# Performance work log

Hardware: AMD Instinct MI355X
Metric: run time of the kernel (lower is better)

The kernel has to match this reference:

```python
import jax, jax.numpy as jnp
import numpy as np

EPS = 1e-5  # torch BatchNorm1d default eps


def setup_inputs() -> dict:
    key = jax.random.key(0)
    ks = jax.random.split(key, 12)
    B, D, H, R, T = 262144, 128, 64, 32, 8
    return {
        "x": jax.random.normal(ks[0], (B, D), dtype=jnp.float32),
        "t": jax.random.randint(ks[1], (B,), 0, T),
        # shared feature net: Linear(D->H), ReLU, BN(H) [eval mode], Dropout(eval=identity)
        "fw": jax.random.normal(ks[2], (H, D), dtype=jnp.float32) * 0.05,
        "fb": jax.random.normal(ks[3], (H,), dtype=jnp.float32) * 0.05,
        "f_gamma": jnp.ones((H,), jnp.float32),
        "f_beta": jnp.zeros((H,), jnp.float32),
        "f_mean": jax.random.normal(ks[4], (H,), dtype=jnp.float32) * 0.05,
        "f_var": jax.random.uniform(ks[5], (H,), minval=0.5, maxval=1.5),
        # T treatment heads, weights stacked on leading axis:
        # Linear(H->R), ReLU, BN(R), Dropout, Linear(R->1)
        "tw1": jax.random.normal(ks[6], (T, R, H), dtype=jnp.float32) * 0.05,
        "tb1": jax.random.normal(ks[7], (T, R), dtype=jnp.float32) * 0.05,
        "t_gamma": jnp.ones((T, R), jnp.float32),
        "t_beta": jnp.zeros((T, R), jnp.float32),
        "t_mean": jax.random.normal(ks[8], (T, R), dtype=jnp.float32) * 0.05,
        "t_var": jax.random.uniform(ks[9], (T, R), minval=0.5, maxval=1.5),
        "tw2": jax.random.normal(ks[10], (T, R), dtype=jnp.float32) * 0.05,  # [T,1,R] squeezed
        "tb2": jax.random.normal(ks[11], (T,), dtype=jnp.float32) * 0.05,
    }


def reference(x, t, fw, fb, f_gamma, f_beta, f_mean, f_var,
              tw1, tb1, t_gamma, t_beta, t_mean, t_var, tw2, tb2):
    # shared representation: Linear -> ReLU -> BN(eval) -> Dropout(identity)
    h = jax.nn.relu(x @ fw.T + fb)                                     # [B,H]
    h = f_gamma * (h - f_mean) * jax.lax.rsqrt(f_var + EPS) + f_beta   # [B,H]
    # run all T tiny heads densely, then select per-sample head (jit-friendly
    # equivalent of the boolean-mask gather/scatter loop; BN is eval-mode so
    # per-group masking and full-batch compute give identical math)
    z = jnp.einsum('bh,trh->btr', h, tw1) + tb1[None]                  # [B,T,R]
    z = jax.nn.relu(z)
    z = t_gamma[None] * (z - t_mean[None]) * jax.lax.rsqrt(t_var[None] + EPS) + t_beta[None]
    out_all = jnp.einsum('btr,tr->bt', z, tw2) + tb2[None]             # [B,T]
    pred = jnp.take_along_axis(out_all, t[:, None], axis=1)            # [B,1]
    return pred
```

## Files before the change

### kernel.cpp

```cpp
#include <hip/hip_runtime.h>
#include <hip/hip_bf16.h>
#include <cstdint>

#define EPS 1e-5f

typedef short bf16x8 __attribute__((ext_vector_type(8)));
typedef float f32x16 __attribute__((ext_vector_type(16)));
typedef unsigned int u32x4 __attribute__((ext_vector_type(4)));

#define WS_TW1S 0
#define WS_FW   8192
#define WS_TB1Q 12288
#define WS_W2Q  12544
#define WS_FBQ  12800
#define WS_C2   12864

static __device__ __forceinline__ unsigned short f2bf(float f) {
    unsigned int u = __float_as_uint(f);
    u += 0x7fffu + ((u >> 16) & 1u);
    return (unsigned short)(u >> 16);
}
static __device__ __forceinline__ short f2bf_fast(float f) {
    __hip_bfloat16 b = __float2bfloat16(f);
    return __builtin_bit_cast(short, b);
}
static __device__ __forceinline__ unsigned pk_bf16(float lo, float hi) {
    unsigned l = (unsigned)(unsigned short)__builtin_bit_cast(unsigned short, __float2bfloat16(lo));
    unsigned h = (unsigned)(unsigned short)__builtin_bit_cast(unsigned short, __float2bfloat16(hi));
    return l | (h << 16);
}

__global__ void tarnet_pre(
    const float* __restrict__ fw, const float* __restrict__ fb,
    const float* __restrict__ f_gamma, const float* __restrict__ f_beta,
    const float* __restrict__ f_mean,  const float* __restrict__ f_var,
    const float* __restrict__ tw1, const float* __restrict__ tb1,
    const float* __restrict__ t_gamma, const float* __restrict__ t_beta,
    const float* __restrict__ t_mean,  const float* __restrict__ t_var,
    const float* __restrict__ tw2, const float* __restrict__ tb2,
    float* __restrict__ ws)
{
    __shared__ float fs[64], fsh[64];
    const int i = threadIdx.x;
    if (i < 64) {
        float s = f_gamma[i] * rsqrtf(f_var[i] + EPS);
        fs[i]  = s;
        fsh[i] = f_beta[i] - f_mean[i] * s;
    }
    __syncthreads();

    unsigned short* tw1s_u = (unsigned short*)(ws + WS_TW1S);
    unsigned short* fw_u   = (unsigned short*)(ws + WS_FW);

    const int t = i >> 5, r = i & 31;
    const int idx = t * 32 + r;
    {
        float tsc  = t_gamma[idx] * rsqrtf(t_var[idx] + EPS);
        float w2s  = tw2[idx] * tsc;
        float tb1s = tb1[idx];
        for (int j = 0; j < 64; ++j) {
            float w = tw1[idx * 64 + j];
            tb1s += w * fsh[j];
            int ht = j >> 5, qq = (j >> 3) & 3, h = (j >> 2) & 1, m = j & 3;
            int ks = ht * 2 + (qq >> 1);
            int ep = (qq & 1) * 4 + m;
            tw1s_u[(((t*4 + ks)*2 + h)*32 + r)*8 + ep] = f2bf(w * fs[j]);
        }
        int q  = ((r >> 3) << 2) | (r & 3);
        int hq = (r >> 2) & 1;
        ws[WS_TB1Q + (t*2 + hq)*16 + q] = tb1s;
        ws[WS_W2Q  + (t*2 + hq)*16 + q] = w2s;
    }
    if (r == 0) {
        float a = tb2[t];
        for (int rr = 0; rr < 32; ++rr) {
            int id2 = t*32 + rr;
            float ts2 = t_gamma[id2] * rsqrtf(t_var[id2] + EPS);
            a += tw2[id2] * (t_beta[id2] - ts2 * t_mean[id2]);
        }
        ws[WS_C2 + t] = a;
    }
    if (i < 64) {
        for (int k = 0; k < 128; ++k) fw_u[i*128 + k] = f2bf(fw[i*128 + k]);
        int ht = i >> 5, r32 = i & 31;
        int q  = ((r32 >> 3) << 2) | (r32 & 3);
        int hq = (r32 >> 2) & 1;
        ws[WS_FBQ + hq*32 + ht*16 + q] = fb[i];
    }
}

__global__ __launch_bounds__(256) void tarnet_main(
    const float* __restrict__ x, const int* __restrict__ t_arr,
    const float* __restrict__ ws, float* __restrict__ out)
{
    const int tid  = threadIdx.x;
    const int wave = tid >> 6, lane = tid & 63;
    const int ln31 = lane & 31, hi = lane >> 5;
    const int swave = blockIdx.x * 256 + wave * 64;

    const unsigned short* fw_u   = (const unsigned short*)(ws + WS_FW);
    const unsigned short* tw1s_u = (const unsigned short*)(ws + WS_TW1S);

    const int tsel0 = t_arr[swave + ln31];
    const int tsel1 = t_arr[swave + 32 + ln31];

    f32x16 acc[2][2];
    {
        float fi2[32];
        const float4* fbq4 = (const float4*)(ws + WS_FBQ);
#pragma unroll
        for (int i2 = 0; i2 < 8; ++i2) {
            float4 v = fbq4[hi*8 + i2];
            fi2[i2*4+0] = v.x; fi2[i2*4+1] = v.y; fi2[i2*4+2] = v.z; fi2[i2*4+3] = v.w;
        }
#pragma unroll
        for (int ht = 0; ht < 2; ++ht)
#pragma unroll
            for (int q = 0; q < 16; ++q) {
                acc[0][ht][q] = fi2[ht*16 + q];
                acc[1][ht][q] = fi2[ht*16 + q];
            }
    }
#pragma unroll
    for (int ks = 0; ks < 8; ++ks) {
        bf16x8 wa0 = *(const bf16x8*)(fw_u + (ln31     )*128 + ks*16 + hi*8);
        bf16x8 wa1 = *(const bf16x8*)(fw_u + (ln31 + 32)*128 + ks*16 + hi*8);
#pragma unroll
        for (int st = 0; st < 2; ++st) {
            const float* xp = x + (size_t)(swave + st*32 + ln31) * 128 + ks*16 + hi*8;
            float4 xa = *(const float4*)xp;
            float4 xb = *(const float4*)(xp + 4);
            bf16x8 xf;
            xf[0] = f2bf_fast(xa.x); xf[1] = f2bf_fast(xa.y);
            xf[2] = f2bf_fast(xa.z); xf[3] = f2bf_fast(xa.w);
            xf[4] = f2bf_fast(xb.x); xf[5] = f2bf_fast(xb.y);
            xf[6] = f2bf_fast(xb.z); xf[7] = f2bf_fast(xb.w);
            acc[st][0] = __builtin_amdgcn_mfma_f32_32x32x16_bf16(wa0, xf, acc[st][0], 0, 0, 0);
            acc[st][1] = __builtin_amdgcn_mfma_f32_32x32x16_bf16(wa1, xf, acc[st][1], 0, 0, 0);
        }
    }

    bf16x8 hb[2][4];
#pragma unroll
    for (int st = 0; st < 2; ++st) {
        unsigned w0[2][4], w1[2][4];
#pragma unroll
        for (int ht = 0; ht < 2; ++ht)
#pragma unroll
            for (int qq = 0; qq < 4; ++qq) {
                float a0 = fmaxf(acc[st][ht][qq*4+0], 0.f);
                float a1 = fmaxf(acc[st][ht][qq*4+1], 0.f);
                float a2 = fmaxf(acc[st][ht][qq*4+2], 0.f);
                float a3 = fmaxf(acc[st][ht][qq*4+3], 0.f);
                w0[ht][qq] = pk_bf16(a0, a1);
                w1[ht][qq] = pk_bf16(a2, a3);
            }
#pragma unroll
        for (int ks = 0; ks < 4; ++ks) {
            const int ht = ks >> 1, qa = (ks & 1) * 2;
            u32x4 wv = {w0[ht][qa], w1[ht][qa], w0[ht][qa+1], w1[ht][qa+1]};
            hb[st][ks] = __builtin_bit_cast(bf16x8, wv);
        }
    }

    float out0 = 0.f, out1 = 0.f;
#pragma unroll 2
    for (int th = 0; th < 8; ++th) {
        bf16x8 aw[4];
#pragma unroll
        for (int ks = 0; ks < 4; ++ks)
            aw[ks] = *(const bf16x8*)(tw1s_u + (((th*4 + ks)*2 + hi)*32 + ln31)*8);
        float4 tb4[4];
#pragma unroll
        for (int i2 = 0; i2 < 4; ++i2)
            tb4[i2] = ((const float4*)(ws + WS_TB1Q))[(th*2 + hi)*4 + i2];
        const float c2t = ws[WS_C2 + th];
#pragma unroll
        for (int st = 0; st < 2; ++st) {
            f32x16 z;
#pragma unroll
            for (int q = 0; q < 16; ++q) z[q] = ((const float*)tb4)[q];
            z = __builtin_amdgcn_mfma_f32_32x32x16_bf16(aw[0], hb[st][0], z, 0, 0, 0);
            z = __builtin_amdgcn_mfma_f32_32x32x16_bf16(aw[1], hb[st][1], z, 0, 0, 0);
            z = __builtin_amdgcn_mfma_f32_32x32x16_bf16(aw[2], hb[st][2], z, 0, 0, 0);
            z = __builtin_amdgcn_mfma_f32_32x32x16_bf16(aw[3], hb[st][3], z, 0, 0, 0);
            float4 w24[4];
#pragma unroll
            for (int i2 = 0; i2 < 4; ++i2)
                w24[i2] = ((const float4*)(ws + WS_W2Q))[(th*2 + hi)*4 + i2];
            float p = 0.f;
#pragma unroll
            for (int q = 0; q < 16; ++q)
                p = fmaf(((const float*)w24)[q], fmaxf(z[q], 0.f), p);
            p += __shfl_xor(p, 32);
            p += c2t;
            if (st == 0) out0 = (th == tsel0) ? p : out0;
            else         out1 = (th == tsel1) ? p : out1;
        }
    }
    out[swave + lane] = hi ? out1 : out0;
}

extern "C" void kernel_launch(void* const* d_in, const int* in_sizes, int n_in,
                              void* d_out, int out_size, void* d_ws, size_t ws_size,
                              hipStream_t stream) {
    const float* x       = (const float*)d_in[0];
    const int*   t       = (const int*)  d_in[1];
    const float* fw      = (const float*)d_in[2];
    const float* fb      = (const float*)d_in[3];
    const float* f_gamma = (const float*)d_in[4];
    const float* f_beta  = (const float*)d_in[5];
    const float* f_mean  = (const float*)d_in[6];
    const float* f_var   = (const float*)d_in[7];
    const float* tw1     = (const float*)d_in[8];
    const float* tb1     = (const float*)d_in[9];
    const float* t_gamma = (const float*)d_in[10];
    const float* t_beta  = (const float*)d_in[11];
    const float* t_mean  = (const float*)d_in[12];
    const float* t_var   = (const float*)d_in[13];
    const float* tw2     = (const float*)d_in[14];
    const float* tb2     = (const float*)d_in[15];

    float* ws   = (float*)d_ws;
    float* outp = (float*)d_out;
    const int B = in_sizes[0] / 128;

    tarnet_pre<<<1, 256, 0, stream>>>(fw, fb, f_gamma, f_beta, f_mean, f_var,
                                      tw1, tb1, t_gamma, t_beta, t_mean, t_var,
                                      tw2, tb2, ws);
    tarnet_main<<<B / 256, 256, 0, stream>>>(x, t, ws, outp);
}
```

Before: 63.47 us.

## Bucket samples by treatment to compute only the selected head

```diff
diff --git a/kernel.cpp b/kernel.cpp
--- a/kernel.cpp
+++ b/kernel.cpp
@@ -14,20 +14,27 @@
 #define WS_W2Q  12544
 #define WS_FBQ  12800
 #define WS_C2   12864
+#define WI_HIST 13056
+#define WI_BASE 21248
+#define WI_CNT  21256
+#define WI_TOT  21264
+#define WI_SORT 21312
+
+#define NBLK 1024
 
 static __device__ __forceinline__ unsigned short f2bf(float f) {
     unsigned int u = __float_as_uint(f);
     u += 0x7fffu + ((u >> 16) & 1u);
     return (unsigned short)(u >> 16);
 }
-static __device__ __forceinline__ short f2bf_fast(float f) {
-    __hip_bfloat16 b = __float2bfloat16(f);
-    return __builtin_bit_cast(short, b);
-}
 static __device__ __forceinline__ unsigned pk_bf16(float lo, float hi) {
     unsigned l = (unsigned)(unsigned short)__builtin_bit_cast(unsigned short, __float2bfloat16(lo));
     unsigned h = (unsigned)(unsigned short)__builtin_bit_cast(unsigned short, __float2bfloat16(hi));
     return l | (h << 16);
+}
+static __device__ __forceinline__ short f2bf_fast(float f) {
+    __hip_bfloat16 b = __float2bfloat16(f);
+    return __builtin_bit_cast(short, b);
 }
 
 __global__ void tarnet_pre(
@@ -89,20 +96,103 @@
     }
 }
 
+__global__ void tarnet_hist(const int* __restrict__ tv, unsigned* __restrict__ wsu) {
+    __shared__ int cw[4][8];
+    const int tid = threadIdx.x, wave = tid >> 6, lane = tid & 63;
+    const int tt = tv[blockIdx.x * 256 + tid];
+#pragma unroll
+    for (int b = 0; b < 8; ++b) {
+        unsigned long long m = __ballot(tt == b);
+        if (lane == 0) cw[wave][b] = __popcll(m);
+    }
+    __syncthreads();
+    if (tid < 8)
+        wsu[WI_HIST + blockIdx.x * 8 + tid] =
+            (unsigned)(cw[0][tid] + cw[1][tid] + cw[2][tid] + cw[3][tid]);
+}
+
+__global__ void tarnet_scan(unsigned* __restrict__ wsu) {
+    __shared__ int S[8][8];
+    __shared__ int cnt_s[8], base_s[8];
+    const int tid = threadIdx.x;
+    const int t = tid & 7, g = tid >> 3;
+    int s = 0;
+    for (int b = g * 128; b < (g + 1) * 128; ++b) s += (int)wsu[WI_HIST + b * 8 + t];
+    S[g][t] = s;
+    __syncthreads();
+    if (tid < 8) {
+        int acc = 0;
+        for (int gg = 0; gg < 8; ++gg) { int v = S[gg][tid]; S[gg][tid] = acc; acc += v; }
+        cnt_s[tid] = acc;
+        wsu[WI_CNT + tid] = (unsigned)acc;
+    }
+    __syncthreads();
+    if (tid == 0) {
+        int acc = 0;
+        for (int b = 0; b < 8; ++b) { base_s[b] = acc; wsu[WI_BASE + b] = (unsigned)acc;
+                                      acc += (cnt_s[b] + 63) & ~63; }
+        wsu[WI_TOT] = (unsigned)acc;
+    }
+    __syncthreads();
+    {
+        int run = base_s[t] + S[g][t];
+        for (int b = g * 128; b < (g + 1) * 128; ++b) {
+            int v = (int)wsu[WI_HIST + b * 8 + t];
+            wsu[WI_HIST + b * 8 + t] = (unsigned)run;
+            run += v;
+        }
+    }
+    if (tid < 8) {
+        int c = cnt_s[tid], p = (c + 63) & ~63;
+        unsigned e = ((unsigned)tid << 24) | 0x80000000u;
+        for (int s2 = c; s2 < p; ++s2) wsu[WI_SORT + base_s[tid] + s2] = e;
+    }
+}
+
+__global__ void tarnet_scatter(const int* __restrict__ tv, unsigned* __restrict__ wsu) {
+    __shared__ int cw[4][8], pw[4][8];
+    const int tid = threadIdx.x, wave = tid >> 6, lane = tid & 63;
+    const int i = blockIdx.x * 256 + tid;
+    const int tt = tv[i];
+    const unsigned long long mlt = (1ull << lane) - 1ull;
+    int prefix = 0;
+#pragma unroll
+    for (int b = 0; b < 8; ++b) {
+        unsigned long long m = __ballot(tt == b);
+        if (tt == b) prefix = __popcll(m & mlt);
+        if (lane == 0) cw[wave][b] = __popcll(m);
+    }
+    __syncthreads();
+    if (tid < 8) {
+        int a = 0;
+        for (int w = 0; w < 4; ++w) { pw[w][tid] = a; a += cw[w][tid]; }
+    }
+    __syncthreads();
+    const int pos = (int)wsu[WI_HIST + blockIdx.x * 8 + tt] + pw[wave][tt] + prefix;
+    wsu[WI_SORT + pos] = (unsigned)i | ((unsigned)tt << 24);
+}
+
 __global__ __launch_bounds__(256) void tarnet_main(
-    const float* __restrict__ x, const int* __restrict__ t_arr,
-    const float* __restrict__ ws, float* __restrict__ out)
+    const float* __restrict__ x, const float* __restrict__ ws,
+    float* __restrict__ out)
 {
     const int tid  = threadIdx.x;
     const int wave = tid >> 6, lane = tid & 63;
     const int ln31 = lane & 31, hi = lane >> 5;
-    const int swave = blockIdx.x * 256 + wave * 64;
+    const unsigned* wsu = (const unsigned*)ws;
+
+    const int total = (int)wsu[WI_TOT];
+    const int gslot = blockIdx.x * 256 + wave * 64;
+    if (gslot >= total) return;
+
+    const unsigned e0 = wsu[WI_SORT + gslot + ln31];
+    const unsigned e1 = wsu[WI_SORT + gslot + 32 + ln31];
+    const int th = (__builtin_amdgcn_readfirstlane((int)e0) >> 24) & 7;
+    const int idx0 = (int)(e0 & 0xFFFFFFu);
+    const int idx1 = (int)(e1 & 0xFFFFFFu);
 
     const unsigned short* fw_u   = (const unsigned short*)(ws + WS_FW);
     const unsigned short* tw1s_u = (const unsigned short*)(ws + WS_TW1S);
-
-    const int tsel0 = t_arr[swave + ln31];
-    const int tsel1 = t_arr[swave + 32 + ln31];
 
     f32x16 acc[2][2];
     {
@@ -127,7 +217,7 @@
         bf16x8 wa1 = *(const bf16x8*)(fw_u + (ln31 + 32)*128 + ks*16 + hi*8);
 #pragma unroll
         for (int st = 0; st < 2; ++st) {
-            const float* xp = x + (size_t)(swave + st*32 + ln31) * 128 + ks*16 + hi*8;
+            const float* xp = x + (size_t)(st ? idx1 : idx0) * 128 + ks*16 + hi*8;
             float4 xa = *(const float4*)xp;
             float4 xb = *(const float4*)(xp + 4);
             bf16x8 xf;
@@ -163,42 +253,36 @@
         }
     }
 
-    float out0 = 0.f, out1 = 0.f;
-#pragma unroll 2
-    for (int th = 0; th < 8; ++th) {
-        bf16x8 aw[4];
-#pragma unroll
-        for (int ks = 0; ks < 4; ++ks)
-            aw[ks] = *(const bf16x8*)(tw1s_u + (((th*4 + ks)*2 + hi)*32 + ln31)*8);
-        float4 tb4[4];
-#pragma unroll
-        for (int i2 = 0; i2 < 4; ++i2)
-            tb4[i2] = ((const float4*)(ws + WS_TB1Q))[(th*2 + hi)*4 + i2];
-        const float c2t = ws[WS_C2 + th];
-#pragma unroll
-        for (int st = 0; st < 2; ++st) {
-            f32x16 z;
-#pragma unroll
-            for (int q = 0; q < 16; ++q) z[q] = ((const float*)tb4)[q];
-            z = __builtin_amdgcn_mfma_f32_32x32x16_bf16(aw[0], hb[st][0], z, 0, 0, 0);
-            z = __builtin_amdgcn_mfma_f32_32x32x16_bf16(aw[1], hb[st][1], z, 0, 0, 0);
-            z = __builtin_amdgcn_mfma_f32_32x32x16_bf16(aw[2], hb[st][2], z, 0, 0, 0);
-            z = __builtin_amdgcn_mfma_f32_32x32x16_bf16(aw[3], hb[st][3], z, 0, 0, 0);
-            float4 w24[4];
-#pragma unroll
-            for (int i2 = 0; i2 < 4; ++i2)
-                w24[i2] = ((const float4*)(ws + WS_W2Q))[(th*2 + hi)*4 + i2];
-            float p = 0.f;
-#pragma unroll
-            for (int q = 0; q < 16; ++q)
-                p = fmaf(((const float*)w24)[q], fmaxf(z[q], 0.f), p);
-            p += __shfl_xor(p, 32);
-            p += c2t;
-            if (st == 0) out0 = (th == tsel0) ? p : out0;
-            else         out1 = (th == tsel1) ? p : out1;
-        }
-    }
-    out[swave + lane] = hi ? out1 : out0;
+    bf16x8 aw[4];
+#pragma unroll
+    for (int ks = 0; ks < 4; ++ks)
+        aw[ks] = *(const bf16x8*)(tw1s_u + (((th*4 + ks)*2 + hi)*32 + ln31)*8);
+    float4 tb4[4], w24[4];
+#pragma unroll
+    for (int i2 = 0; i2 < 4; ++i2) {
+        tb4[i2] = ((const float4*)(ws + WS_TB1Q))[(th*2 + hi)*4 + i2];
+        w24[i2] = ((const float4*)(ws + WS_W2Q))[(th*2 + hi)*4 + i2];
+    }
+    const float c2t = ws[WS_C2 + th];
+
+#pragma unroll
+    for (int st = 0; st < 2; ++st) {
+        f32x16 z;
+#pragma unroll
+        for (int q = 0; q < 16; ++q) z[q] = ((const float*)tb4)[q];
+        z = __builtin_amdgcn_mfma_f32_32x32x16_bf16(aw[0], hb[st][0], z, 0, 0, 0);
+        z = __builtin_amdgcn_mfma_f32_32x32x16_bf16(aw[1], hb[st][1], z, 0, 0, 0);
+        z = __builtin_amdgcn_mfma_f32_32x32x16_bf16(aw[2], hb[st][2], z, 0, 0, 0);
+        z = __builtin_amdgcn_mfma_f32_32x32x16_bf16(aw[3], hb[st][3], z, 0, 0, 0);
+        float p = 0.f;
+#pragma unroll
+        for (int q = 0; q < 16; ++q)
+            p = fmaf(((const float*)w24)[q], fmaxf(z[q], 0.f), p);
+        p += __shfl_xor(p, 32);
+        p += c2t;
+        const unsigned e = st ? e1 : e0;
+        if (!(e & 0x80000000u)) out[st ? idx1 : idx0] = p;
+    }
 }
 
 extern "C" void kernel_launch(void* const* d_in, const int* in_sizes, int n_in,
@@ -221,12 +305,17 @@
     const float* tw2     = (const float*)d_in[14];
     const float* tb2     = (const float*)d_in[15];
 
-    float* ws   = (float*)d_ws;
-    float* outp = (float*)d_out;
+    float*    ws   = (float*)d_ws;
+    unsigned* wsu  = (unsigned*)d_ws;
+    float*    outp = (float*)d_out;
     const int B = in_sizes[0] / 128;
 
     tarnet_pre<<<1, 256, 0, stream>>>(fw, fb, f_gamma, f_beta, f_mean, f_var,
                                       tw1, tb1, t_gamma, t_beta, t_mean, t_var,
                                       tw2, tb2, ws);
-    tarnet_main<<<B / 256, 256, 0, stream>>>(x, t, ws, outp);
-}
+    tarnet_hist<<<B / 256, 256, 0, stream>>>(t, wsu);
+    tarnet_scan<<<1, 64, 0, stream>>>(wsu);
+    tarnet_scatter<<<B / 256, 256, 0, stream>>>(t, wsu);
+    const int grid = (B + 8 * 64 + 255) / 256;
+    tarnet_main<<<grid, 256, 0, stream>>>(x, ws, outp);
+}
```

Result: slower. 65.48 us (+3.2%).

## Halve per-wave sample tile and preload full x row into registers

Applied to the files above, without the earlier changes.

```diff
diff --git a/kernel.cpp b/kernel.cpp
--- a/kernel.cpp
+++ b/kernel.cpp
@@ -20,14 +20,14 @@
     u += 0x7fffu + ((u >> 16) & 1u);
     return (unsigned short)(u >> 16);
 }
-static __device__ __forceinline__ short f2bf_fast(float f) {
-    __hip_bfloat16 b = __float2bfloat16(f);
-    return __builtin_bit_cast(short, b);
-}
 static __device__ __forceinline__ unsigned pk_bf16(float lo, float hi) {
     unsigned l = (unsigned)(unsigned short)__builtin_bit_cast(unsigned short, __float2bfloat16(lo));
     unsigned h = (unsigned)(unsigned short)__builtin_bit_cast(unsigned short, __float2bfloat16(hi));
     return l | (h << 16);
+}
+static __device__ __forceinline__ short f2bf_fast(float f) {
+    __hip_bfloat16 b = __float2bfloat16(f);
+    return __builtin_bit_cast(short, b);
 }
 
 __global__ void tarnet_pre(
@@ -89,69 +89,64 @@
     }
 }
 
-__global__ __launch_bounds__(256) void tarnet_main(
+__global__ __launch_bounds__(256, 4) void tarnet_main(
     const float* __restrict__ x, const int* __restrict__ t_arr,
     const float* __restrict__ ws, float* __restrict__ out)
 {
     const int tid  = threadIdx.x;
     const int wave = tid >> 6, lane = tid & 63;
     const int ln31 = lane & 31, hi = lane >> 5;
-    const int swave = blockIdx.x * 256 + wave * 64;
+    const int sample = blockIdx.x * 128 + wave * 32 + ln31;
 
     const unsigned short* fw_u   = (const unsigned short*)(ws + WS_FW);
     const unsigned short* tw1s_u = (const unsigned short*)(ws + WS_TW1S);
 
-    const int tsel0 = t_arr[swave + ln31];
-    const int tsel1 = t_arr[swave + 32 + ln31];
-
-    f32x16 acc[2][2];
+    const int tsel = t_arr[sample];
+
+    float4 xr[16];
+    const float4* xp = (const float4*)x + (size_t)sample * 32 + hi * 2;
+#pragma unroll
+    for (int ks = 0; ks < 8; ++ks) {
+        xr[2*ks]   = xp[ks*4];
+        xr[2*ks+1] = xp[ks*4 + 1];
+    }
+
+    f32x16 acc[2];
     {
-        float fi2[32];
         const float4* fbq4 = (const float4*)(ws + WS_FBQ);
 #pragma unroll
         for (int i2 = 0; i2 < 8; ++i2) {
             float4 v = fbq4[hi*8 + i2];
-            fi2[i2*4+0] = v.x; fi2[i2*4+1] = v.y; fi2[i2*4+2] = v.z; fi2[i2*4+3] = v.w;
-        }
-#pragma unroll
-        for (int ht = 0; ht < 2; ++ht)
-#pragma unroll
-            for (int q = 0; q < 16; ++q) {
-                acc[0][ht][q] = fi2[ht*16 + q];
-                acc[1][ht][q] = fi2[ht*16 + q];
-            }
+            const int ht = i2 >> 2, qb = (i2 & 3) * 4;
+            acc[ht][qb+0] = v.x; acc[ht][qb+1] = v.y;
+            acc[ht][qb+2] = v.z; acc[ht][qb+3] = v.w;
+        }
     }
 #pragma unroll
     for (int ks = 0; ks < 8; ++ks) {
         bf16x8 wa0 = *(const bf16x8*)(fw_u + (ln31     )*128 + ks*16 + hi*8);
         bf16x8 wa1 = *(const bf16x8*)(fw_u + (ln31 + 32)*128 + ks*16 + hi*8);
-#pragma unroll
-        for (int st = 0; st < 2; ++st) {
-            const float* xp = x + (size_t)(swave + st*32 + ln31) * 128 + ks*16 + hi*8;
-            float4 xa = *(const float4*)xp;
-            float4 xb = *(const float4*)(xp + 4);
-            bf16x8 xf;
-            xf[0] = f2bf_fast(xa.x); xf[1] = f2bf_fast(xa.y);
-            xf[2] = f2bf_fast(xa.z); xf[3] = f2bf_fast(xa.w);
-            xf[4] = f2bf_fast(xb.x); xf[5] = f2bf_fast(xb.y);
-            xf[6] = f2bf_fast(xb.z); xf[7] = f2bf_fast(xb.w);
-            acc[st][0] = __builtin_amdgcn_mfma_f32_32x32x16_bf16(wa0, xf, acc[st][0], 0, 0, 0);
-            acc[st][1] = __builtin_amdgcn_mfma_f32_32x32x16_bf16(wa1, xf, acc[st][1], 0, 0, 0);
-        }
-    }
-
-    bf16x8 hb[2][4];
-#pragma unroll
-    for (int st = 0; st < 2; ++st) {
+        float4 xa = xr[2*ks], xb = xr[2*ks+1];
+        bf16x8 xf;
+        xf[0] = f2bf_fast(xa.x); xf[1] = f2bf_fast(xa.y);
+        xf[2] = f2bf_fast(xa.z); xf[3] = f2bf_fast(xa.w);
+        xf[4] = f2bf_fast(xb.x); xf[5] = f2bf_fast(xb.y);
+        xf[6] = f2bf_fast(xb.z); xf[7] = f2bf_fast(xb.w);
+        acc[0] = __builtin_amdgcn_mfma_f32_32x32x16_bf16(wa0, xf, acc[0], 0, 0, 0);
+        acc[1] = __builtin_amdgcn_mfma_f32_32x32x16_bf16(wa1, xf, acc[1], 0, 0, 0);
+    }
+
+    bf16x8 hb[4];
+    {
         unsigned w0[2][4], w1[2][4];
 #pragma unroll
         for (int ht = 0; ht < 2; ++ht)
 #pragma unroll
             for (int qq = 0; qq < 4; ++qq) {
-                float a0 = fmaxf(acc[st][ht][qq*4+0], 0.f);
-                float a1 = fmaxf(acc[st][ht][qq*4+1], 0.f);
-                float a2 = fmaxf(acc[st][ht][qq*4+2], 0.f);
-                float a3 = fmaxf(acc[st][ht][qq*4+3], 0.f);
+                float a0 = fmaxf(acc[ht][qq*4+0], 0.f);
+                float a1 = fmaxf(acc[ht][qq*4+1], 0.f);
+                float a2 = fmaxf(acc[ht][qq*4+2], 0.f);
+                float a3 = fmaxf(acc[ht][qq*4+3], 0.f);
                 w0[ht][qq] = pk_bf16(a0, a1);
                 w1[ht][qq] = pk_bf16(a2, a3);
             }
@@ -159,46 +154,40 @@
         for (int ks = 0; ks < 4; ++ks) {
             const int ht = ks >> 1, qa = (ks & 1) * 2;
             u32x4 wv = {w0[ht][qa], w1[ht][qa], w0[ht][qa+1], w1[ht][qa+1]};
-            hb[st][ks] = __builtin_bit_cast(bf16x8, wv);
-        }
-    }
-
-    float out0 = 0.f, out1 = 0.f;
+            hb[ks] = __builtin_bit_cast(bf16x8, wv);
+        }
+    }
+
+    float outv = 0.f;
 #pragma unroll 2
     for (int th = 0; th < 8; ++th) {
         bf16x8 aw[4];
 #pragma unroll
         for (int ks = 0; ks < 4; ++ks)
             aw[ks] = *(const bf16x8*)(tw1s_u + (((th*4 + ks)*2 + hi)*32 + ln31)*8);
-        float4 tb4[4];
-#pragma unroll
-        for (int i2 = 0; i2 < 4; ++i2)
+        float4 tb4[4], w24[4];
+#pragma unroll
+        for (int i2 = 0; i2 < 4; ++i2) {
             tb4[i2] = ((const float4*)(ws + WS_TB1Q))[(th*2 + hi)*4 + i2];
+            w24[i2] = ((const float4*)(ws + WS_W2Q))[(th*2 + hi)*4 + i2];
+        }
         const float c2t = ws[WS_C2 + th];
-#pragma unroll
-        for (int st = 0; st < 2; ++st) {
-            f32x16 z;
-#pragma unroll
-            for (int q = 0; q < 16; ++q) z[q] = ((const float*)tb4)[q];
-            z = __builtin_amdgcn_mfma_f32_32x32x16_bf16(aw[0], hb[st][0], z, 0, 0, 0);
-            z = __builtin_amdgcn_mfma_f32_32x32x16_bf16(aw[1], hb[st][1], z, 0, 0, 0);
-            z = __builtin_amdgcn_mfma_f32_32x32x16_bf16(aw[2], hb[st][2], z, 0, 0, 0);
-            z = __builtin_amdgcn_mfma_f32_32x32x16_bf16(aw[3], hb[st][3], z, 0, 0, 0);
-            float4 w24[4];
-#pragma unroll
-            for (int i2 = 0; i2 < 4; ++i2)
-                w24[i2] = ((const float4*)(ws + WS_W2Q))[(th*2 + hi)*4 + i2];
-            float p = 0.f;
-#pragma unroll
-            for (int q = 0; q < 16; ++q)
-                p = fmaf(((const float*)w24)[q], fmaxf(z[q], 0.f), p);
-            p += __shfl_xor(p, 32);
-            p += c2t;
-            if (st == 0) out0 = (th == tsel0) ? p : out0;
-            else         out1 = (th == tsel1) ? p : out1;
-        }
-    }
-    out[swave + lane] = hi ? out1 : out0;
+        f32x16 z;
+#pragma unroll
+        for (int q = 0; q < 16; ++q) z[q] = ((const float*)tb4)[q];
+        z = __builtin_amdgcn_mfma_f32_32x32x16_bf16(aw[0], hb[0], z, 0, 0, 0);
+        z = __builtin_amdgcn_mfma_f32_32x32x16_bf16(aw[1], hb[1], z, 0, 0, 0);
+        z = __builtin_amdgcn_mfma_f32_32x32x16_bf16(aw[2], hb[2], z, 0, 0, 0);
+        z = __builtin_amdgcn_mfma_f32_32x32x16_bf16(aw[3], hb[3], z, 0, 0, 0);
+        float p = 0.f;
+#pragma unroll
+        for (int q = 0; q < 16; ++q)
+            p = fmaf(((const float*)w24)[q], fmaxf(z[q], 0.f), p);
+        p += __shfl_xor(p, 32);
+        p += c2t;
+        outv = (th == tsel) ? p : outv;
+    }
+    if (!hi) out[sample] = outv;
 }
 
 extern "C" void kernel_launch(void* const* d_in, const int* in_sizes, int n_in,
@@ -228,5 +217,5 @@
     tarnet_pre<<<1, 256, 0, stream>>>(fw, fb, f_gamma, f_beta, f_mean, f_var,
                                       tw1, tb1, t_gamma, t_beta, t_mean, t_var,
                                       tw2, tb2, ws);
-    tarnet_main<<<B / 256, 256, 0, stream>>>(x, t, ws, outp);
-}
+    tarnet_main<<<B / 128, 256, 0, stream>>>(x, t, ws, outp);
+}
```

Result: slower. 71.73 us (+13.0%).

## Stage preprocessed weights in LDS and prefetch all x rows upfront

Applied to the files above, without the earlier changes.

```diff
diff --git a/kernel.cpp b/kernel.cpp
--- a/kernel.cpp
+++ b/kernel.cpp
@@ -9,25 +9,26 @@
 typedef unsigned int u32x4 __attribute__((ext_vector_type(4)));
 
 #define WS_TW1S 0
-#define WS_FW   8192
+#define WS_FWQ  8192
 #define WS_TB1Q 12288
 #define WS_W2Q  12544
 #define WS_FBQ  12800
 #define WS_C2   12864
+#define WS_TOTAL 12872
 
 static __device__ __forceinline__ unsigned short f2bf(float f) {
     unsigned int u = __float_as_uint(f);
     u += 0x7fffu + ((u >> 16) & 1u);
     return (unsigned short)(u >> 16);
 }
-static __device__ __forceinline__ short f2bf_fast(float f) {
-    __hip_bfloat16 b = __float2bfloat16(f);
-    return __builtin_bit_cast(short, b);
-}
 static __device__ __forceinline__ unsigned pk_bf16(float lo, float hi) {
     unsigned l = (unsigned)(unsigned short)__builtin_bit_cast(unsigned short, __float2bfloat16(lo));
     unsigned h = (unsigned)(unsigned short)__builtin_bit_cast(unsigned short, __float2bfloat16(hi));
     return l | (h << 16);
+}
+static __device__ __forceinline__ short f2bf_fast(float f) {
+    __hip_bfloat16 b = __float2bfloat16(f);
+    return __builtin_bit_cast(short, b);
 }
 
 __global__ void tarnet_pre(
@@ -50,7 +51,7 @@
     __syncthreads();
 
     unsigned short* tw1s_u = (unsigned short*)(ws + WS_TW1S);
-    unsigned short* fw_u   = (unsigned short*)(ws + WS_FW);
+    unsigned short* fwq_u  = (unsigned short*)(ws + WS_FWQ);
 
     const int t = i >> 5, r = i & 31;
     const int idx = t * 32 + r;
@@ -81,7 +82,10 @@
         ws[WS_C2 + t] = a;
     }
     if (i < 64) {
-        for (int k = 0; k < 128; ++k) fw_u[i*128 + k] = f2bf(fw[i*128 + k]);
+        for (int k = 0; k < 128; ++k) {
+            int ks = k >> 4, h = (k >> 3) & 1, jj = k & 7;
+            fwq_u[(((ks*2 + h)*64) + i)*8 + jj] = f2bf(fw[i*128 + k]);
+        }
         int ht = i >> 5, r32 = i & 31;
         int q  = ((r32 >> 3) << 2) | (r32 & 3);
         int hq = (r32 >> 2) & 1;
@@ -89,55 +93,76 @@
     }
 }
 
-__global__ __launch_bounds__(256) void tarnet_main(
+__global__ __launch_bounds__(256, 2) void tarnet_main(
     const float* __restrict__ x, const int* __restrict__ t_arr,
     const float* __restrict__ ws, float* __restrict__ out)
 {
+    __shared__ float smem[WS_TOTAL];
+    {
+        const uint4* src = (const uint4*)ws;
+        uint4* dst = (uint4*)smem;
+        for (int k = threadIdx.x; k < WS_TOTAL / 4; k += 256) dst[k] = src[k];
+    }
+    __syncthreads();
+
+    const unsigned short* s_tw1s = (const unsigned short*)smem;
+    const unsigned short* s_fwq  = (const unsigned short*)(smem + WS_FWQ);
+    const float* s_tb1q = smem + WS_TB1Q;
+    const float* s_w2q  = smem + WS_W2Q;
+    const float* s_fbq  = smem + WS_FBQ;
+    const float* s_c2   = smem + WS_C2;
+
     const int tid  = threadIdx.x;
     const int wave = tid >> 6, lane = tid & 63;
     const int ln31 = lane & 31, hi = lane >> 5;
-    const int swave = blockIdx.x * 256 + wave * 64;
-
-    const unsigned short* fw_u   = (const unsigned short*)(ws + WS_FW);
-    const unsigned short* tw1s_u = (const unsigned short*)(ws + WS_TW1S);
-
-    const int tsel0 = t_arr[swave + ln31];
-    const int tsel1 = t_arr[swave + 32 + ln31];
+    const int sbase = blockIdx.x * 256 + wave * 64;
+
+    const int tsel0 = t_arr[sbase + ln31];
+    const int tsel1 = t_arr[sbase + 32 + ln31];
+
+    float4 xr[32];
+    {
+        const float4* xq0 = (const float4*)x + (size_t)(sbase + ln31) * 32 + hi * 2;
+        const float4* xq1 = (const float4*)x + (size_t)(sbase + 32 + ln31) * 32 + hi * 2;
+#pragma unroll
+        for (int ks = 0; ks < 8; ++ks) {
+            xr[2*ks]      = xq0[ks*4];
+            xr[2*ks+1]    = xq0[ks*4 + 1];
+            xr[16+2*ks]   = xq1[ks*4];
+            xr[16+2*ks+1] = xq1[ks*4 + 1];
+        }
+    }
+    bf16x8 xb[16];
+#pragma unroll
+    for (int i2 = 0; i2 < 16; ++i2) {
+        float4 xa = xr[2*i2], xc = xr[2*i2+1];
+        bf16x8 v;
+        v[0] = f2bf_fast(xa.x); v[1] = f2bf_fast(xa.y);
+        v[2] = f2bf_fast(xa.z); v[3] = f2bf_fast(xa.w);
+        v[4] = f2bf_fast(xc.x); v[5] = f2bf_fast(xc.y);
+        v[6] = f2bf_fast(xc.z); v[7] = f2bf_fast(xc.w);
+        xb[i2] = v;
+    }
 
     f32x16 acc[2][2];
     {
-        float fi2[32];
-        const float4* fbq4 = (const float4*)(ws + WS_FBQ);
-#pragma unroll
-        for (int i2 = 0; i2 < 8; ++i2) {
-            float4 v = fbq4[hi*8 + i2];
-            fi2[i2*4+0] = v.x; fi2[i2*4+1] = v.y; fi2[i2*4+2] = v.z; fi2[i2*4+3] = v.w;
-        }
 #pragma unroll
         for (int ht = 0; ht < 2; ++ht)
 #pragma unroll
             for (int q = 0; q < 16; ++q) {
-                acc[0][ht][q] = fi2[ht*16 + q];
-                acc[1][ht][q] = fi2[ht*16 + q];
+                float v = s_fbq[hi*32 + ht*16 + q];
+                acc[0][ht][q] = v;
+                acc[1][ht][q] = v;
             }
     }
 #pragma unroll
     for (int ks = 0; ks < 8; ++ks) {
-        bf16x8 wa0 = *(const bf16x8*)(fw_u + (ln31     )*128 + ks*16 + hi*8);
-        bf16x8 wa1 = *(const bf16x8*)(fw_u + (ln31 + 32)*128 + ks*16 + hi*8);
-#pragma unroll
-        for (int st = 0; st < 2; ++st) {
-            const float* xp = x + (size_t)(swave + st*32 + ln31) * 128 + ks*16 + hi*8;
-            float4 xa = *(const float4*)xp;
-            float4 xb = *(const float4*)(xp + 4);
-            bf16x8 xf;
-            xf[0] = f2bf_fast(xa.x); xf[1] = f2bf_fast(xa.y);
-            xf[2] = f2bf_fast(xa.z); xf[3] = f2bf_fast(xa.w);
-            xf[4] = f2bf_fast(xb.x); xf[5] = f2bf_fast(xb.y);
-            xf[6] = f2bf_fast(xb.z); xf[7] = f2bf_fast(xb.w);
-            acc[st][0] = __builtin_amdgcn_mfma_f32_32x32x16_bf16(wa0, xf, acc[st][0], 0, 0, 0);
-            acc[st][1] = __builtin_amdgcn_mfma_f32_32x32x16_bf16(wa1, xf, acc[st][1], 0, 0, 0);
-        }
+        bf16x8 wa0 = *(const bf16x8*)(s_fwq + (((ks*2 + hi)*64) + ln31     )*8);
+        bf16x8 wa1 = *(const bf16x8*)(s_fwq + (((ks*2 + hi)*64) + ln31 + 32)*8);
+        acc[0][0] = __builtin_amdgcn_mfma_f32_32x32x16_bf16(wa0, xb[ks],   acc[0][0], 0, 0, 0);
+        acc[0][1] = __builtin_amdgcn_mfma_f32_32x32x16_bf16(wa1, xb[ks],   acc[0][1], 0, 0, 0);
+        acc[1][0] = __builtin_amdgcn_mfma_f32_32x32x16_bf16(wa0, xb[8+ks], acc[1][0], 0, 0, 0);
+        acc[1][1] = __builtin_amdgcn_mfma_f32_32x32x16_bf16(wa1, xb[8+ks], acc[1][1], 0, 0, 0);
     }
 
     bf16x8 hb[2][4];
@@ -169,36 +194,35 @@
         bf16x8 aw[4];
 #pragma unroll
         for (int ks = 0; ks < 4; ++ks)
-            aw[ks] = *(const bf16x8*)(tw1s_u + (((th*4 + ks)*2 + hi)*32 + ln31)*8);
-        float4 tb4[4];
-#pragma unroll
-        for (int i2 = 0; i2 < 4; ++i2)
-            tb4[i2] = ((const float4*)(ws + WS_TB1Q))[(th*2 + hi)*4 + i2];
-        const float c2t = ws[WS_C2 + th];
+            aw[ks] = *(const bf16x8*)(s_tw1s + (((th*4 + ks)*2 + hi)*32 + ln31)*8);
+        const float* tbq = s_tb1q + (th*2 + hi)*16;
+        const float* w2q = s_w2q  + (th*2 + hi)*16;
+        const float c2t  = s_c2[th];
 #pragma unroll
         for (int st = 0; st < 2; ++st) {
             f32x16 z;
 #pragma unroll
-            for (int q = 0; q < 16; ++q) z[q] = ((const float*)tb4)[q];
+            for (int q = 0; q < 16; ++q) z[q] = tbq[q];
             z = __builtin_amdgcn_mfma_f32_32x32x16_bf16(aw[0], hb[st][0], z, 0, 0, 0);
             z = __builtin_amdgcn_mfma_f32_32x32x16_bf16(aw[1], hb[st][1], z, 0, 0, 0);
             z = __builtin_amdgcn_mfma_f32_32x32x16_bf16(aw[2], hb[st][2], z, 0, 0, 0);
             z = __builtin_amdgcn_mfma_f32_32x32x16_bf16(aw[3], hb[st][3], z, 0, 0, 0);
-            float4 w24[4];
-#pragma unroll
-            for (int i2 = 0; i2 < 4; ++i2)
-                w24[i2] = ((const float4*)(ws + WS_W2Q))[(th*2 + hi)*4 + i2];
-            float p = 0.f;
-#pragma unroll
-            for (int q = 0; q < 16; ++q)
-                p = fmaf(((const float*)w24)[q], fmaxf(z[q], 0.f), p);
+            float p0 = 0.f, p1 = 0.f, p2 = 0.f, p3 = 0.f;
+#pragma unroll
+            for (int q = 0; q < 4; ++q) {
+                p0 = fmaf(w2q[q],    fmaxf(z[q],    0.f), p0);
+                p1 = fmaf(w2q[q+4],  fmaxf(z[q+4],  0.f), p1);
+                p2 = fmaf(w2q[q+8],  fmaxf(z[q+8],  0.f), p2);
+                p3 = fmaf(w2q[q+12], fmaxf(z[q+12], 0.f), p3);
+            }
+            float p = (p0 + p1) + (p2 + p3);
             p += __shfl_xor(p, 32);
             p += c2t;
             if (st == 0) out0 = (th == tsel0) ? p : out0;
             else         out1 = (th == tsel1) ? p : out1;
         }
     }
-    out[swave + lane] = hi ? out1 : out0;
+    out[sbase + lane] = hi ? out1 : out0;
 }
 
 extern "C" void kernel_launch(void* const* d_in, const int* in_sizes, int n_in,
```

Result: no change. 63.15 us (-0.5%).
